# Kernel optimization log

Hardware: AMD Instinct MI355X
Metric: run time of the kernel (lower is better)

Reference implementation:

```python
import jax, jax.numpy as jnp
import numpy as np

NUM_EMBEDDINGS = 512
EMBEDDING_DIM = 100
COMMITMENT_COST = 0.25


def setup_inputs() -> dict:
    key = jax.random.key(0)
    k1, k2 = jax.random.split(key)
    inputs = jax.random.normal(k1, (64, 64, 64, EMBEDDING_DIM), dtype=jnp.float32)
    # nn.Embedding weight init: uniform(-1/num_embeddings, 1/num_embeddings)
    lim = 1.0 / NUM_EMBEDDINGS
    embedding = jax.random.uniform(k2, (NUM_EMBEDDINGS, EMBEDDING_DIM),
                                   dtype=jnp.float32, minval=-lim, maxval=lim)
    return {"inputs": inputs, "embedding": embedding}


def reference(inputs, embedding):
    d = inputs.shape[-1]
    flat = inputs.reshape(-1, d)                                  # [N, d]
    # squared L2 distances to each codebook entry: [N, K]
    distances = (jnp.sum(flat ** 2, axis=1, keepdims=True)
                 + jnp.sum(embedding ** 2, axis=1)
                 - 2.0 * flat @ embedding.T)
    encoding_indices = jnp.argmin(distances, axis=1)              # [N]
    quantized = embedding[encoding_indices].reshape(inputs.shape)
    commitment_loss = COMMITMENT_COST * jnp.mean(
        (jax.lax.stop_gradient(quantized) - inputs) ** 2)
    quantization_loss = jnp.mean(
        (quantized - jax.lax.stop_gradient(inputs)) ** 2)
    # straight-through estimator
    quantized_st = inputs + jax.lax.stop_gradient(quantized - inputs)
    return quantized_st, quantization_loss, commitment_loss
```

## Files before the change

### kernel.cpp

```cpp
#include <hip/hip_runtime.h>
#include <hip/hip_bf16.h>
#include <cfloat>


#define N_ROWS (64 * 64 * 64)
#define D 100
#define KCODES 512
#define CB_OFF 4096
#define E2_OFF 16

typedef __attribute__((ext_vector_type(8))) short short8;
typedef __attribute__((ext_vector_type(4))) float f32x4;

__device__ __forceinline__ unsigned short f2bf(float f) {
    union { float f; unsigned u; } v; v.f = f;
    unsigned r = v.u + 0x7FFF + ((v.u >> 16) & 1);
    return (unsigned short)(r >> 16);
}
__device__ __forceinline__ unsigned pk2(float a, float b) {
    union { __hip_bfloat162 h; unsigned u; } c;
    c.h = __float22bfloat162_rn(make_float2(a, b));
    return c.u;
}
__device__ __forceinline__ short8 pack8(const float4& a, const float4& b) {
    union { unsigned u[4]; short8 v; } r;
    r.u[0] = pk2(a.x, a.y); r.u[1] = pk2(a.z, a.w);
    r.u[2] = pk2(b.x, b.y); r.u[3] = pk2(b.z, b.w);
    return r.v;
}

__global__ __launch_bounds__(64) void vq_init(const float* __restrict__ emb,
                                              float* __restrict__ ws) {
    const int code = blockIdx.x, l = threadIdx.x;
    const float* e = emb + code * D;
    if (code == 0 && l == 0) ws[0] = 0.0f;
    float a = e[l];
    float b = (l < D - 64) ? e[64 + l] : 0.0f;
    float p = fmaf(a, a, b * b);
#pragma unroll
    for (int off = 32; off; off >>= 1) p += __shfl_xor(p, off);
    if (l == 0) ws[E2_OFF + code] = p;

    if (l < 16) {
        const int s = l >> 2, q = l & 3;
        short8 v;
#pragma unroll
        for (int j = 0; j < 8; ++j) {
            int k = s * 32 + q * 8 + j;
            v[j] = (k < D) ? (short)f2bf(e[k]) : (short)0;
        }
        const int chunk = code >> 5, ci = code & 31;
        const int tt = ci >> 4, lr = ci & 15;
        unsigned short* cb = (unsigned short*)((char*)ws + CB_OFF);
        *(short8*)(cb + chunk * 4096 + ((s * 2 + tt) * 64 + q * 16 + lr) * 8) = v;
    }
}

__global__ __launch_bounds__(512, 2) void vq_main(const float* __restrict__ x,
                                                  const float* __restrict__ emb,
                                                  float* __restrict__ ws,
                                                  float* __restrict__ out) {
    __shared__ uint4  bbuf[2][512];
    __shared__ float  e2s[KCODES];
    __shared__ int    widx[512];
    __shared__ float  wsum[8];

    const int tid = threadIdx.x, wave = tid >> 6, lane = tid & 63;
    const int quad = lane >> 4, lr = lane & 15;
    const long brow = (long)blockIdx.x * 512;
    const long wrow = brow + wave * 64;

    float4 av[4][7];
#pragma unroll
    for (int m = 0; m < 4; ++m) {
        const float* xr = x + (wrow + m * 16 + lr) * D + quad * 8;
        av[m][0] = *(const float4*)(xr);
        av[m][1] = *(const float4*)(xr + 4);
        av[m][2] = *(const float4*)(xr + 32);
        av[m][3] = *(const float4*)(xr + 36);
        av[m][4] = *(const float4*)(xr + 64);
        av[m][5] = *(const float4*)(xr + 68);
        av[m][6] = *(const float4*)(x + (wrow + m * 16 + lr) * D + 96);
    }

    const uint4* __restrict__ cbg = (const uint4*)((const char*)ws + CB_OFF);
    uint4 st0 = cbg[tid];
    const float* __restrict__ e2g = ws + E2_OFF;
    e2s[tid] = e2g[tid];

    short8 A[4][4];
    float  xnorm[4];
#pragma unroll
    for (int m = 0; m < 4; ++m) {
        float4 z = av[m][6];
        if (quad != 0) z = make_float4(0.f, 0.f, 0.f, 0.f);
        float nrm = 0.f;
#pragma unroll
        for (int i = 0; i < 6; ++i) {
            float4 f = av[m][i];
            nrm = fmaf(f.x, f.x, nrm); nrm = fmaf(f.y, f.y, nrm);
            nrm = fmaf(f.z, f.z, nrm); nrm = fmaf(f.w, f.w, nrm);
        }
        nrm = fmaf(z.x, z.x, nrm); nrm = fmaf(z.y, z.y, nrm);
        nrm = fmaf(z.z, z.z, nrm); nrm = fmaf(z.w, z.w, nrm);
        A[m][0] = pack8(av[m][0], av[m][1]);
        A[m][1] = pack8(av[m][2], av[m][3]);
        A[m][2] = pack8(av[m][4], av[m][5]);
        A[m][3] = pack8(z, make_float4(0.f, 0.f, 0.f, 0.f));
        nrm += __shfl_xor(nrm, 16);
        nrm += __shfl_xor(nrm, 32);
        xnorm[m] = nrm;
    }

    bbuf[0][tid] = st0;
    __syncthreads();

    float    runmin[4][4];
    unsigned runidx[4][4];
#pragma unroll
    for (int m = 0; m < 4; ++m)
#pragma unroll
        for (int r = 0; r < 4; ++r) { runmin[m][r] = FLT_MAX; runidx[m][r] = 0; }

    for (int c = 0; c < 16; ++c) {
        const int p = c & 1;
        uint4 n0;
        if (c < 15) n0 = cbg[(c + 1) * 512 + tid];

        const short8* __restrict__ bl = (const short8*)&bbuf[p][0];
        short8 B[2][4];
#pragma unroll
        for (int s = 0; s < 4; ++s) {
            B[0][s] = bl[(s * 2 + 0) * 64 + lane];
            B[1][s] = bl[(s * 2 + 1) * 64 + lane];
        }
        float e2v0 = e2s[c * 32 + lr];
        float e2v1 = e2s[c * 32 + 16 + lr];

        f32x4 acc[4][2];
#pragma unroll
        for (int m = 0; m < 4; ++m) {
            acc[m][0] = (f32x4){0.f, 0.f, 0.f, 0.f};
            acc[m][1] = (f32x4){0.f, 0.f, 0.f, 0.f};
        }
#pragma unroll
        for (int s = 0; s < 4; ++s)
#pragma unroll
            for (int m = 0; m < 4; ++m) {
                acc[m][0] = __builtin_amdgcn_mfma_f32_16x16x32_bf16(A[m][s], B[0][s], acc[m][0], 0, 0, 0);
                acc[m][1] = __builtin_amdgcn_mfma_f32_16x16x32_bf16(A[m][s], B[1][s], acc[m][1], 0, 0, 0);
            }

#pragma unroll
        for (int m = 0; m < 4; ++m)
#pragma unroll
            for (int tt = 0; tt < 2; ++tt) {
                float e2v = tt ? e2v1 : e2v0;
                unsigned code = c * 32 + tt * 16 + lr;
#pragma unroll
                for (int r = 0; r < 4; ++r) {
                    float sc = fmaf(-2.0f, acc[m][tt][r], e2v);
                    if (sc < runmin[m][r]) { runmin[m][r] = sc; runidx[m][r] = code; }
                }
            }

        if (c < 15) bbuf[p ^ 1][tid] = n0;
        __syncthreads();
    }

    float lsum = 0.0f;
#pragma unroll
    for (int m = 0; m < 4; ++m)
#pragma unroll
        for (int r = 0; r < 4; ++r) {
            float    s = runmin[m][r];
            unsigned i = runidx[m][r];
#pragma unroll
            for (int off = 8; off >= 1; off >>= 1) {
                float    os = __shfl_xor(s, off);
                unsigned oi = (unsigned)__shfl_xor((int)i, off);
                if (os < s || (os == s && oi < i)) { s = os; i = oi; }
            }
            if (lr == quad * 4 + r) {
                lsum += xnorm[m] + s;
                widx[wave * 64 + m * 16 + quad * 4 + r] = (int)i;
            }
        }
#pragma unroll
    for (int off = 32; off >= 1; off >>= 1) lsum += __shfl_xor(lsum, off);
    if (lane == 0) wsum[wave] = lsum;
    __syncthreads();
    if (tid == 0) {
        float t = 0.f;
#pragma unroll
        for (int w = 0; w < 8; ++w) t += wsum[w];
        atomicAdd(ws, t);
    }

    const float4* __restrict__ ef = (const float4*)emb;
    float4* __restrict__ og = (float4*)(out + brow * D);
#pragma unroll
    for (int i = 0; i < 25; i += 5) {
        float4 q[5];
        int    gi[5];
#pragma unroll
        for (int u = 0; u < 5; ++u) {
            int g = (i + u) * 512 + tid;
            int row = g / 25;
            int c4  = g - row * 25;
            gi[u] = g;
            q[u]  = ef[(long)widx[row] * 25 + c4];
        }
#pragma unroll
        for (int u = 0; u < 5; ++u) og[gi[u]] = q[u];
    }
}

__global__ void vq_final(const float* __restrict__ ws, float* __restrict__ out) {
    float mse = ws[0] / (float)((long)N_ROWS * D);
    out[(long)N_ROWS * D]     = mse;
    out[(long)N_ROWS * D + 1] = 0.25f * mse;
}

extern "C" void kernel_launch(void* const* d_in, const int* in_sizes, int n_in,
                              void* d_out, int out_size, void* d_ws, size_t ws_size,
                              hipStream_t stream) {
    const float* x   = (const float*)d_in[0];
    const float* emb = (const float*)d_in[1];
    float* out = (float*)d_out;
    float* ws  = (float*)d_ws;

    vq_init<<<KCODES, 64, 0, stream>>>(emb, ws);
    vq_main<<<N_ROWS / 512, 512, 0, stream>>>(x, emb, ws, out);
    vq_final<<<1, 1, 0, stream>>>(ws, out);
}
```

Before: 237.9 us.

## Stage full codebook in LDS once and drop per-chunk block barriers

Each block now copies the whole bf16 codebook (128 KB) into shared memory at the start, instead of double-buffering one 8 KB chunk per iteration. This removes the per-chunk global load and the __syncthreads in the distance loop. The loss reduction now does one atomic per wave into 8 slots that the final kernel sums, replacing the block-level shared reduction and its barrier. The gather/store epilogue becomes per-wave so no block barrier is needed. The cost is roughly 135 KB of LDS per block, which allows only one 512-thread block per CU instead of two, and adds a large serialized codebook load per block.

```diff
diff --git a/kernel.cpp b/kernel.cpp
--- a/kernel.cpp
+++ b/kernel.cpp
@@ -33,7 +33,7 @@
                                               float* __restrict__ ws) {
     const int code = blockIdx.x, l = threadIdx.x;
     const float* e = emb + code * D;
-    if (code == 0 && l == 0) ws[0] = 0.0f;
+    if (code == 0 && l < 8) ws[l] = 0.0f;
     float a = e[l];
     float b = (l < D - 64) ? e[64 + l] : 0.0f;
     float p = fmaf(a, a, b * b);
@@ -60,10 +60,9 @@
                                                   const float* __restrict__ emb,
                                                   float* __restrict__ ws,
                                                   float* __restrict__ out) {
-    __shared__ uint4  bbuf[2][512];
+    __shared__ uint4  sbuf[8192];
     __shared__ float  e2s[KCODES];
     __shared__ int    widx[512];
-    __shared__ float  wsum[8];
 
     const int tid = threadIdx.x, wave = tid >> 6, lane = tid & 63;
     const int quad = lane >> 4, lr = lane & 15;
@@ -84,8 +83,18 @@
     }
 
     const uint4* __restrict__ cbg = (const uint4*)((const char*)ws + CB_OFF);
-    uint4 st0 = cbg[tid];
     const float* __restrict__ e2g = ws + E2_OFF;
+#pragma unroll
+    for (int kk = 0; kk < 16; kk += 4) {
+        uint4 t0 = cbg[(kk + 0) * 512 + tid];
+        uint4 t1 = cbg[(kk + 1) * 512 + tid];
+        uint4 t2 = cbg[(kk + 2) * 512 + tid];
+        uint4 t3 = cbg[(kk + 3) * 512 + tid];
+        sbuf[(kk + 0) * 512 + tid] = t0;
+        sbuf[(kk + 1) * 512 + tid] = t1;
+        sbuf[(kk + 2) * 512 + tid] = t2;
+        sbuf[(kk + 3) * 512 + tid] = t3;
+    }
     e2s[tid] = e2g[tid];
 
     short8 A[4][4];
@@ -112,7 +121,6 @@
         xnorm[m] = nrm;
     }
 
-    bbuf[0][tid] = st0;
     __syncthreads();
 
     float    runmin[4][4];
@@ -122,17 +130,14 @@
 #pragma unroll
         for (int r = 0; r < 4; ++r) { runmin[m][r] = FLT_MAX; runidx[m][r] = 0; }
 
+    const short8* __restrict__ sbl = (const short8*)sbuf;
+
     for (int c = 0; c < 16; ++c) {
-        const int p = c & 1;
-        uint4 n0;
-        if (c < 15) n0 = cbg[(c + 1) * 512 + tid];
-
-        const short8* __restrict__ bl = (const short8*)&bbuf[p][0];
         short8 B[2][4];
 #pragma unroll
         for (int s = 0; s < 4; ++s) {
-            B[0][s] = bl[(s * 2 + 0) * 64 + lane];
-            B[1][s] = bl[(s * 2 + 1) * 64 + lane];
+            B[0][s] = sbl[c * 512 + (s * 2 + 0) * 64 + lane];
+            B[1][s] = sbl[c * 512 + (s * 2 + 1) * 64 + lane];
         }
         float e2v0 = e2s[c * 32 + lr];
         float e2v1 = e2s[c * 32 + 16 + lr];
@@ -163,9 +168,6 @@
                     if (sc < runmin[m][r]) { runmin[m][r] = sc; runidx[m][r] = code; }
                 }
             }
-
-        if (c < 15) bbuf[p ^ 1][tid] = n0;
-        __syncthreads();
     }
 
     float lsum = 0.0f;
@@ -188,28 +190,24 @@
         }
 #pragma unroll
     for (int off = 32; off >= 1; off >>= 1) lsum += __shfl_xor(lsum, off);
-    if (lane == 0) wsum[wave] = lsum;
-    __syncthreads();
-    if (tid == 0) {
-        float t = 0.f;
-#pragma unroll
-        for (int w = 0; w < 8; ++w) t += wsum[w];
-        atomicAdd(ws, t);
-    }
+    if (lane == 0) atomicAdd(&ws[wave], lsum);
+
+    asm volatile("s_waitcnt lgkmcnt(0)" ::: "memory");
 
     const float4* __restrict__ ef = (const float4*)emb;
-    float4* __restrict__ og = (float4*)(out + brow * D);
+    float4* __restrict__ og = (float4*)(out + wrow * D);
+    const int rbase = wave * 64;
 #pragma unroll
     for (int i = 0; i < 25; i += 5) {
         float4 q[5];
         int    gi[5];
 #pragma unroll
         for (int u = 0; u < 5; ++u) {
-            int g = (i + u) * 512 + tid;
+            int g = (i + u) * 64 + lane;
             int row = g / 25;
             int c4  = g - row * 25;
             gi[u] = g;
-            q[u]  = ef[(long)widx[row] * 25 + c4];
+            q[u]  = ef[(long)widx[rbase + row] * 25 + c4];
         }
 #pragma unroll
         for (int u = 0; u < 5; ++u) og[gi[u]] = q[u];
@@ -217,7 +215,10 @@
 }
 
 __global__ void vq_final(const float* __restrict__ ws, float* __restrict__ out) {
-    float mse = ws[0] / (float)((long)N_ROWS * D);
+    float t = 0.f;
+#pragma unroll
+    for (int w = 0; w < 8; ++w) t += ws[w];
+    float mse = t / (float)((long)N_ROWS * D);
     out[(long)N_ROWS * D]     = mse;
     out[(long)N_ROWS * D + 1] = 0.25f * mse;
 }
```

Result: slower. 261.9 us (+10.1%).
